# Optimization experiments

Hardware: AMD Instinct MI355X
Metric: run time of the kernel (lower is better)

## Reference

```python
import jax, jax.numpy as jnp
import numpy as np

NUM_HEADS = 16
EMBED_DIM = 2048
HEAD_DIM = EMBED_DIM // NUM_HEADS
B, S = 2, 2048


def setup_inputs() -> dict:
    key = jax.random.key(0)
    ks = jax.random.split(key, 12)
    E = EMBED_DIM
    scale = 1.0 / np.sqrt(E)  # xavier-ish for square E->E dense
    inp = {
        "x": jax.random.normal(ks[0], (B, S, E), dtype=jnp.float32),
        "sin": jax.random.uniform(ks[1], (1, NUM_HEADS, S, HEAD_DIM), dtype=jnp.float32),
        "cos": jax.random.uniform(ks[2], (1, NUM_HEADS, S, HEAD_DIM), dtype=jnp.float32),
        "mask": jax.random.randint(ks[3], (B, S, S), 0, 2, dtype=jnp.int32),
        "Wq": jax.random.normal(ks[4], (E, E), dtype=jnp.float32) * scale,
        "bq": jnp.zeros((E,), dtype=jnp.float32),
        "Wk": jax.random.normal(ks[5], (E, E), dtype=jnp.float32) * scale,
        "bk": jnp.zeros((E,), dtype=jnp.float32),
        "Wv": jax.random.normal(ks[6], (E, E), dtype=jnp.float32) * scale,
        "bv": jnp.zeros((E,), dtype=jnp.float32),
        "Wo": jax.random.normal(ks[7], (E, E), dtype=jnp.float32) * scale,
        "bo": jnp.zeros((E,), dtype=jnp.float32),
    }
    return inp


def _minus_swap_alternate(t):
    # stack([-t[...,1::2], t[...,::2]], -1).reshape(t.shape)
    return jnp.stack([-t[..., 1::2], t[..., ::2]], axis=-1).reshape(t.shape)


def _forward(x, sin, cos, mask, Wq, bq, Wk, bk, Wv, bv, Wo, bo):
    Bx, Sx, E = x.shape
    H, D = NUM_HEADS, HEAD_DIM
    q = (x @ Wq + bq).reshape(Bx, Sx, H, D).transpose(0, 2, 1, 3)  # (B,H,S,D)
    k = (x @ Wk + bk).reshape(Bx, Sx, H, D).transpose(0, 2, 1, 3)
    v = (x @ Wv + bv).reshape(Bx, Sx, H, D).transpose(0, 2, 1, 3)
    # RoPE applied post-transpose: T = q.shape[1] == H (faithful to source)
    T = q.shape[1]
    s = sin[:, :T, :, :]
    c = cos[:, :T, :, :]
    q = q * c + _minus_swap_alternate(q) * s
    k = k * c + _minus_swap_alternate(k) * s
    m = mask[:, None, :, :]  # expand_mask: (B,S,S) -> (B,1,S,S)
    logits = jnp.einsum("bhqd,bhkd->bhqk", q, k) / jnp.sqrt(jnp.float32(D))
    logits = jnp.where(m == 0, jnp.float32(-9e15), logits)
    attention = jax.nn.softmax(logits, axis=-1)          # first softmax
    values = jnp.matmul(attention, v)                    # (B,H,S,D)
    attention_weights = jax.nn.softmax(attention, axis=-1)  # redundant second softmax
    attn_output = jnp.matmul(attention_weights, values)  # (B,H,S,D)
    attn_output = attn_output.transpose(0, 2, 1, 3).reshape(Bx, Sx, E)
    out = attn_output @ Wo + bo
    return out, attention_weights


def reference(x, sin, cos, mask, Wq, bq, Wk, bk, Wv, bv, Wo, bo):
    return _forward(x, sin, cos, mask, Wq, bq, Wk, bk, Wv, bv, Wo, bo)
```

## Files before the change

kernel.cpp:

```cpp
#include <hip/hip_runtime.h>

typedef unsigned short u16;
typedef unsigned int u32;
typedef __attribute__((ext_vector_type(8))) short short8;
typedef __attribute__((ext_vector_type(4))) float floatx4;

constexpr int Bc = 2, Sc = 2048, Ec = 2048, Hc = 16, Dc = 128;
constexpr int TILE = 128, BK = 32;

__device__ __forceinline__ u16 f2bf(float f) {
  u32 u = __builtin_bit_cast(u32, f);
  u = (u + 0x7FFFu + ((u >> 16) & 1u)) >> 16;
  return (u16)u;
}

__device__ __forceinline__ short8 pack2(float4 a, float4 b) {
  short8 r;
  r[0] = (short)f2bf(a.x); r[1] = (short)f2bf(a.y);
  r[2] = (short)f2bf(a.z); r[3] = (short)f2bf(a.w);
  r[4] = (short)f2bf(b.x); r[5] = (short)f2bf(b.y);
  r[6] = (short)f2bf(b.z); r[7] = (short)f2bf(b.w);
  return r;
}

__device__ __forceinline__ void glds16(const u16* g, u16* l) {
  __builtin_amdgcn_global_load_lds(
      (const __attribute__((address_space(1))) u32*)g,
      (__attribute__((address_space(3))) u32*)l, 16, 0, 0);
}

__device__ __forceinline__ void gemm_core(const u16* __restrict__ A, int lda,
                                          const u16* __restrict__ Bt, int ldb,
                                          int K, int m0, int n0,
                                          u16* smA, u16* smB,
                                          floatx4 (*acc)[4]) {
  const int t = threadIdx.x;
  const int lane = t & 63;
  const int w = t >> 6;
  const int wr = (w >> 1) * 64, wc = (w & 1) * 64;
  const int l15 = lane & 15, q = lane >> 4;

  const int r0 = t >> 2;
  const int c0 = (t & 3) ^ (r0 & 3);
  const u16* A0 = A + (size_t)(m0 + r0) * lda + c0 * 8;
  const u16* A1 = A0 + (size_t)64 * lda;
  const u16* B0 = Bt + (size_t)(n0 + r0) * ldb + c0 * 8;
  const u16* B1 = B0 + (size_t)64 * ldb;
  u16* dA0 = smA + w * 512;
  u16* dA1 = smA + 2048 + w * 512;
  u16* dB0 = smB + w * 512;
  u16* dB1 = smB + 2048 + w * 512;

  for (int k0 = 0; k0 < K; k0 += BK) {
    glds16(A0 + k0, dA0);
    glds16(A1 + k0, dA1);
    glds16(B0 + k0, dB0);
    glds16(B1 + k0, dB1);
    __syncthreads();

    short8 af[4], bfr[4];
    #pragma unroll
    for (int i = 0; i < 4; i++) {
      int ra = wr + i * 16 + l15;
      af[i] = *(const short8*)&smA[ra * BK + ((q ^ (ra & 3)) << 3)];
      int rb = wc + i * 16 + l15;
      bfr[i] = *(const short8*)&smB[rb * BK + ((q ^ (rb & 3)) << 3)];
    }
    #pragma unroll
    for (int mi = 0; mi < 4; mi++)
      #pragma unroll
      for (int ni = 0; ni < 4; ni++)
        acc[mi][ni] = __builtin_amdgcn_mfma_f32_16x16x32_bf16(af[mi], bfr[ni], acc[mi][ni], 0, 0, 0);
    __syncthreads();
  }
}

__global__ __launch_bounds__(256) void transpose_w(
    const float* __restrict__ Wq, const float* __restrict__ Wk,
    const float* __restrict__ Wv, const float* __restrict__ Wo,
    u16* __restrict__ WT, u16* __restrict__ WoT) {
  __shared__ float tile[32][33];
  const int z = blockIdx.z;
  const float* W = (z == 0) ? Wq : (z == 1) ? Wk : (z == 2) ? Wv : Wo;
  u16* dst = (z < 3) ? (WT + (size_t)z * Ec * Ec) : WoT;
  const int n0 = blockIdx.x * 32, k0 = blockIdx.y * 32;
  const int tx = threadIdx.x, ty = threadIdx.y;
  #pragma unroll
  for (int i = 0; i < 4; i++)
    tile[ty + 8 * i][tx] = W[(size_t)(k0 + ty + 8 * i) * Ec + n0 + tx];
  __syncthreads();
  #pragma unroll
  for (int i = 0; i < 4; i++)
    dst[(size_t)(n0 + ty + 8 * i) * Ec + k0 + tx] = f2bf(tile[tx][ty + 8 * i]);
}

__global__ __launch_bounds__(256) void xcvt_kernel(const float* __restrict__ x,
                                                   u16* __restrict__ xb,
                                                   float* __restrict__ s1) {
  const int i = blockIdx.x * 256 + threadIdx.x;
  const float4 f0 = ((const float4*)x)[(size_t)i * 2];
  const float4 f1 = ((const float4*)x)[(size_t)i * 2 + 1];
  *(short8*)&xb[(size_t)i * 8] = pack2(f0, f1);
  if (blockIdx.x < 64)
    ((float4*)s1)[i] = make_float4(0.f, 0.f, 0.f, 0.f);
}

__global__ __launch_bounds__(256) void qkv_kernel(
    const u16* __restrict__ xb, const u16* __restrict__ WT,
    const float* __restrict__ bq, const float* __restrict__ bk, const float* __restrict__ bv,
    const float* __restrict__ sinp, const float* __restrict__ cosp,
    u16* __restrict__ qr, u16* __restrict__ kr, u16* __restrict__ vT) {
  __shared__ __align__(16) u16 smA[TILE * BK];
  __shared__ __align__(16) u16 smB[TILE * BK];
  floatx4 acc[4][4] = {};
  const int m0 = blockIdx.y * TILE, n0 = blockIdx.x * TILE;
  gemm_core(xb, Ec, WT, Ec, Ec, m0, n0, smA, smB, acc);

  const int t = threadIdx.x, lane = t & 63, w = t >> 6;
  const int wr = (w >> 1) * 64, wc = (w & 1) * 64, l15 = lane & 15, q = lane >> 4;
  #pragma unroll
  for (int mi = 0; mi < 4; mi++) {
    #pragma unroll
    for (int ni = 0; ni < 4; ni++) {
      const int gcol = n0 + wc + ni * 16 + l15;
      const int which = gcol >> 11;
      const int e = gcol & 2047, h = e >> 7, d = e & 127;
      const float* bp = (which == 0) ? bq : (which == 1) ? bk : bv;
      const float bias = bp[e];
      #pragma unroll
      for (int rr = 0; rr < 4; rr++) {
        const int grow = m0 + wr + mi * 16 + q * 4 + rr;
        const int b = grow >> 11, s = grow & 2047;
        float val = acc[mi][ni][rr] + bias;
        float pv = __shfl_xor(val, 1);
        if (which < 2) {
          const size_t sc = ((size_t)h * Sc + s) * Dc + d;
          const float c = cosp[sc], sn = sinp[sc];
          const float o = val * c + ((d & 1) ? pv : -pv) * sn;
          u16* dst = which ? kr : qr;
          dst[(((size_t)b * Hc + h) * Sc + s) * Dc + d] = f2bf(o);
        } else {
          vT[(((size_t)b * Hc + h) * Dc + d) * Sc + s] = f2bf(val);
        }
      }
    }
  }
}

__global__ __launch_bounds__(256) void logits_kernel(
    const u16* __restrict__ qr, const u16* __restrict__ kr,
    const int* __restrict__ maskp, float* __restrict__ Lo, float* __restrict__ s1) {
  __shared__ __align__(16) u16 smA[TILE * BK];
  __shared__ __align__(16) u16 smB[TILE * BK];
  floatx4 acc[4][4] = {};
  const int z = blockIdx.z;
  const int m0 = blockIdx.y * TILE, n0 = blockIdx.x * TILE;
  gemm_core(qr + (size_t)z * Sc * Dc, Dc, kr + (size_t)z * Sc * Dc, Dc, Dc, m0, n0, smA, smB, acc);

  float* C = Lo + (size_t)z * Sc * Sc;
  const int b = z >> 4;
  const float scale = 0.08838834764831845f;
  const int t = threadIdx.x, lane = t & 63, w = t >> 6;
  const int wr = (w >> 1) * 64, wc = (w & 1) * 64, l15 = lane & 15, q = lane >> 4;
  float rs[4][4];
  #pragma unroll
  for (int mi = 0; mi < 4; mi++)
    #pragma unroll
    for (int rr = 0; rr < 4; rr++) rs[mi][rr] = 0.f;

  #pragma unroll
  for (int mi = 0; mi < 4; mi++)
    #pragma unroll
    for (int ni = 0; ni < 4; ni++) {
      const int gcol = n0 + wc + ni * 16 + l15;
      #pragma unroll
      for (int rr = 0; rr < 4; rr++) {
        const int grow = m0 + wr + mi * 16 + q * 4 + rr;
        const int mv = maskp[((size_t)b * Sc + grow) * Sc + gcol];
        const float val = mv ? acc[mi][ni][rr] * scale : -9.0e15f;
        C[(size_t)grow * Sc + gcol] = val;
        rs[mi][rr] += __expf(val);
      }
    }
  #pragma unroll
  for (int mi = 0; mi < 4; mi++)
    #pragma unroll
    for (int rr = 0; rr < 4; rr++) {
      float xs = rs[mi][rr];
      xs += __shfl_xor(xs, 1);
      xs += __shfl_xor(xs, 2);
      xs += __shfl_xor(xs, 4);
      xs += __shfl_xor(xs, 8);
      if (l15 == 0)
        atomicAdd(&s1[z * Sc + m0 + wr + mi * 16 + q * 4 + rr], xs);
    }
}

__global__ __launch_bounds__(256) void av_kernel(
    const float* __restrict__ L, const u16* __restrict__ vT,
    const float* __restrict__ s1, u16* __restrict__ valT, float* __restrict__ s2) {
  __shared__ __align__(16) u16 smA[TILE * BK];
  __shared__ __align__(16) u16 smB[TILE * BK];
  floatx4 acc[4][4] = {};
  const int z = blockIdx.z;
  const int m0 = blockIdx.y * TILE;
  const int t = threadIdx.x;
  const int r = t >> 1, cg = (t & 1) * 2, sw = r & 3;
  const int lane = t & 63, w = t >> 6;
  const int wr = (w >> 1) * 64, wc = (w & 1) * 64;
  const int l15 = lane & 15, q = lane >> 4;

  const int r0 = t >> 2;
  const int c0 = (t & 3) ^ (r0 & 3);
  const u16* Bb = vT + (size_t)z * Dc * Sc;
  const u16* B0 = Bb + (size_t)r0 * Sc + c0 * 8;
  const u16* B1 = B0 + (size_t)64 * Sc;
  u16* dB0 = smB + w * 512;
  u16* dB1 = smB + 2048 + w * 512;

  const float* Arow = L + (size_t)z * Sc * Sc + (size_t)(m0 + r) * Sc + cg * 8;
  const float inv1 = 1.0f / s1[z * Sc + m0 + r];
  float s2p = 0.0f;

  for (int k0 = 0; k0 < Sc; k0 += BK) {
    glds16(B0 + k0, dB0);
    glds16(B1 + k0, dB1);

    float4 f[4];
    #pragma unroll
    for (int j = 0; j < 4; j++) f[j] = ((const float4*)(Arow + k0))[j];
    #pragma unroll
    for (int j = 0; j < 4; j++) {
      float* e = (float*)&f[j];
      #pragma unroll
      for (int u = 0; u < 4; u++) {
        float a1 = __expf(e[u]) * inv1;
        s2p += __expf(a1);
        e[u] = a1;
      }
    }
    short8 a0 = pack2(f[0], f[1]);
    short8 a1v = pack2(f[2], f[3]);
    *(short8*)&smA[r * BK + (((cg + 0) ^ sw) << 3)] = a0;
    *(short8*)&smA[r * BK + (((cg + 1) ^ sw) << 3)] = a1v;
    __syncthreads();

    short8 af[4], bfr[4];
    #pragma unroll
    for (int i = 0; i < 4; i++) {
      int ra = wr + i * 16 + l15;
      af[i] = *(const short8*)&smA[ra * BK + ((q ^ (ra & 3)) << 3)];
      int rb = wc + i * 16 + l15;
      bfr[i] = *(const short8*)&smB[rb * BK + ((q ^ (rb & 3)) << 3)];
    }
    #pragma unroll
    for (int mi = 0; mi < 4; mi++)
      #pragma unroll
      for (int ni = 0; ni < 4; ni++)
        acc[mi][ni] = __builtin_amdgcn_mfma_f32_16x16x32_bf16(af[mi], bfr[ni], acc[mi][ni], 0, 0, 0);
    __syncthreads();
  }

  float o = __shfl_xor(s2p, 1);
  if ((t & 1) == 0) s2[z * Sc + m0 + r] = s2p + o;

  u16* C = valT + (size_t)z * Dc * Sc;
  #pragma unroll
  for (int mi = 0; mi < 4; mi++)
    #pragma unroll
    for (int ni = 0; ni < 4; ni++) {
      const int gcol = wc + ni * 16 + l15;
      #pragma unroll
      for (int rr = 0; rr < 4; rr++) {
        const int grow = m0 + wr + mi * 16 + q * 4 + rr;
        C[(size_t)gcol * Sc + grow] = f2bf(acc[mi][ni][rr]);
      }
    }
}

__global__ __launch_bounds__(256) void wv_kernel(
    float* __restrict__ L, const u16* __restrict__ valT,
    const float* __restrict__ s1, const float* __restrict__ s2,
    u16* __restrict__ aox) {
  __shared__ __align__(16) u16 smA[TILE * BK];
  __shared__ __align__(16) u16 smB[TILE * BK];
  floatx4 acc[4][4] = {};
  const int z = blockIdx.z;
  const int m0 = blockIdx.y * TILE;
  const int t = threadIdx.x;
  const int r = t >> 1, cg = (t & 1) * 2, sw = r & 3;
  const int lane = t & 63, w = t >> 6;
  const int wr = (w >> 1) * 64, wc = (w & 1) * 64;
  const int l15 = lane & 15, q = lane >> 4;

  const int r0 = t >> 2;
  const int c0 = (t & 3) ^ (r0 & 3);
  const u16* Bb = valT + (size_t)z * Dc * Sc;
  const u16* B0 = Bb + (size_t)r0 * Sc + c0 * 8;
  const u16* B1 = B0 + (size_t)64 * Sc;
  u16* dB0 = smB + w * 512;
  u16* dB1 = smB + 2048 + w * 512;

  float* Arow = L + (size_t)z * Sc * Sc + (size_t)(m0 + r) * Sc + cg * 8;
  const float inv1 = 1.0f / s1[z * Sc + m0 + r];
  const float inv2 = 1.0f / s2[z * Sc + m0 + r];

  for (int k0 = 0; k0 < Sc; k0 += BK) {
    glds16(B0 + k0, dB0);
    glds16(B1 + k0, dB1);

    float4 f[4];
    #pragma unroll
    for (int j = 0; j < 4; j++) f[j] = ((const float4*)(Arow + k0))[j];
    #pragma unroll
    for (int j = 0; j < 4; j++) {
      float* e = (float*)&f[j];
      #pragma unroll
      for (int u = 0; u < 4; u++) {
        float a1 = __expf(e[u]) * inv1;
        e[u] = __expf(a1) * inv2;
      }
    }
    #pragma unroll
    for (int j = 0; j < 4; j++) ((float4*)(Arow + k0))[j] = f[j];
    short8 a0 = pack2(f[0], f[1]);
    short8 a1v = pack2(f[2], f[3]);
    *(short8*)&smA[r * BK + (((cg + 0) ^ sw) << 3)] = a0;
    *(short8*)&smA[r * BK + (((cg + 1) ^ sw) << 3)] = a1v;
    __syncthreads();

    short8 af[4], bfr[4];
    #pragma unroll
    for (int i = 0; i < 4; i++) {
      int ra = wr + i * 16 + l15;
      af[i] = *(const short8*)&smA[ra * BK + ((q ^ (ra & 3)) << 3)];
      int rb = wc + i * 16 + l15;
      bfr[i] = *(const short8*)&smB[rb * BK + ((q ^ (rb & 3)) << 3)];
    }
    #pragma unroll
    for (int mi = 0; mi < 4; mi++)
      #pragma unroll
      for (int ni = 0; ni < 4; ni++)
        acc[mi][ni] = __builtin_amdgcn_mfma_f32_16x16x32_bf16(af[mi], bfr[ni], acc[mi][ni], 0, 0, 0);
    __syncthreads();
  }

  const int b = z >> 4, h = z & 15;
  #pragma unroll
  for (int mi = 0; mi < 4; mi++)
    #pragma unroll
    for (int ni = 0; ni < 4; ni++) {
      const int gcol = wc + ni * 16 + l15;
      #pragma unroll
      for (int rr = 0; rr < 4; rr++) {
        const int grow = m0 + wr + mi * 16 + q * 4 + rr;
        aox[((size_t)b * Sc + grow) * Ec + h * Dc + gcol] = f2bf(acc[mi][ni][rr]);
      }
    }
}

__global__ __launch_bounds__(256) void out_kernel(
    const u16* __restrict__ aox, const u16* __restrict__ WoT,
    const float* __restrict__ bo, float* __restrict__ outp) {
  __shared__ __align__(16) u16 smA[TILE * BK];
  __shared__ __align__(16) u16 smB[TILE * BK];
  floatx4 acc[4][4] = {};
  const int m0 = blockIdx.y * TILE, n0 = blockIdx.x * TILE;
  gemm_core(aox, Ec, WoT, Ec, Ec, m0, n0, smA, smB, acc);

  const int t = threadIdx.x, lane = t & 63, w = t >> 6;
  const int wr = (w >> 1) * 64, wc = (w & 1) * 64, l15 = lane & 15, q = lane >> 4;
  #pragma unroll
  for (int mi = 0; mi < 4; mi++)
    #pragma unroll
    for (int ni = 0; ni < 4; ni++) {
      const int gcol = n0 + wc + ni * 16 + l15;
      const float bias = bo[gcol];
      #pragma unroll
      for (int rr = 0; rr < 4; rr++) {
        const int grow = m0 + wr + mi * 16 + q * 4 + rr;
        outp[(size_t)grow * Ec + gcol] = acc[mi][ni][rr] + bias;
      }
    }
}

extern "C" void kernel_launch(void* const* d_in, const int* in_sizes, int n_in,
                              void* d_out, int out_size, void* d_ws, size_t ws_size,
                              hipStream_t stream) {
  const float* x     = (const float*)d_in[0];
  const float* sinp  = (const float*)d_in[1];
  const float* cosp  = (const float*)d_in[2];
  const int*   maskp = (const int*)d_in[3];
  const float* Wq    = (const float*)d_in[4];
  const float* bq    = (const float*)d_in[5];
  const float* Wk    = (const float*)d_in[6];
  const float* bk    = (const float*)d_in[7];
  const float* Wv    = (const float*)d_in[8];
  const float* bv    = (const float*)d_in[9];
  const float* Wo    = (const float*)d_in[10];
  const float* bo    = (const float*)d_in[11];

  float* out0  = (float*)d_out;
  float* attnL = out0 + (size_t)Bc * Sc * Ec;

  u16* wsp  = (u16*)d_ws;
  u16* WT   = wsp;
  u16* WoT  = WT + (size_t)3 * Ec * Ec;
  u16* xb   = WoT + (size_t)Ec * Ec;
  u16* qr   = xb + (size_t)Bc * Sc * Ec;
  u16* kr   = qr + (size_t)Bc * Hc * Sc * Dc;
  u16* vT   = kr + (size_t)Bc * Hc * Sc * Dc;
  u16* valT = vT + (size_t)Bc * Hc * Sc * Dc;
  u16* aox  = valT + (size_t)Bc * Hc * Sc * Dc;
  float* s1 = (float*)(aox + (size_t)Bc * Sc * Ec);
  float* s2 = s1 + (size_t)Bc * Hc * Sc;

  transpose_w<<<dim3(64, 64, 4), dim3(32, 8), 0, stream>>>(Wq, Wk, Wv, Wo, WT, WoT);
  xcvt_kernel<<<dim3(4096), 256, 0, stream>>>(x, xb, s1);
  qkv_kernel<<<dim3(48, 32), 256, 0, stream>>>(xb, WT, bq, bk, bv, sinp, cosp, qr, kr, vT);
  logits_kernel<<<dim3(16, 16, 32), 256, 0, stream>>>(qr, kr, maskp, attnL, s1);
  av_kernel<<<dim3(1, 16, 32), 256, 0, stream>>>(attnL, vT, s1, valT, s2);
  wv_kernel<<<dim3(1, 16, 32), 256, 0, stream>>>(attnL, valT, s1, s2, aox);
  out_kernel<<<dim3(16, 32), 256, 0, stream>>>(aox, WoT, bo, out0);
}
```

Baseline: 1.466 ms.

## Store unnormalized exp scores as bf16 and defer softmax normalization to epilogue

The logits kernel now writes exp(logit) as bf16 into a workspace buffer instead of fp32 logits into the output. av_kernel loads this buffer straight into LDS with global_load_lds, multiplies by unnormalized P and applies 1/s1 in the epilogue, which removes the per-element exp work from its staging path. wv_kernel reads the bf16 buffer and writes the final fp32 attention weights. This halves the intermediate read traffic at the cost of an extra workspace buffer and bf16 rounding of exp values before normalization and the second softmax.

After: 1.304 ms. 11.0% less time.

```diff
diff --git a/kernel.cpp b/kernel.cpp
--- a/kernel.cpp
+++ b/kernel.cpp
@@ -12,6 +12,11 @@
   u32 u = __builtin_bit_cast(u32, f);
   u = (u + 0x7FFFu + ((u >> 16) & 1u)) >> 16;
   return (u16)u;
+}
+
+__device__ __forceinline__ float bf2f(short s) {
+  u32 u = ((u32)(u16)s) << 16;
+  return __builtin_bit_cast(float, u);
 }
 
 __device__ __forceinline__ short8 pack2(float4 a, float4 b) {
@@ -149,7 +154,7 @@
 
 __global__ __launch_bounds__(256) void logits_kernel(
     const u16* __restrict__ qr, const u16* __restrict__ kr,
-    const int* __restrict__ maskp, float* __restrict__ Lo, float* __restrict__ s1) {
+    const int* __restrict__ maskp, u16* __restrict__ Pbuf, float* __restrict__ s1) {
   __shared__ __align__(16) u16 smA[TILE * BK];
   __shared__ __align__(16) u16 smB[TILE * BK];
   floatx4 acc[4][4] = {};
@@ -157,7 +162,7 @@
   const int m0 = blockIdx.y * TILE, n0 = blockIdx.x * TILE;
   gemm_core(qr + (size_t)z * Sc * Dc, Dc, kr + (size_t)z * Sc * Dc, Dc, Dc, m0, n0, smA, smB, acc);
 
-  float* C = Lo + (size_t)z * Sc * Sc;
+  u16* Pp = Pbuf + (size_t)z * Sc * Sc;
   const int b = z >> 4;
   const float scale = 0.08838834764831845f;
   const int t = threadIdx.x, lane = t & 63, w = t >> 6;
@@ -178,8 +183,9 @@
         const int grow = m0 + wr + mi * 16 + q * 4 + rr;
         const int mv = maskp[((size_t)b * Sc + grow) * Sc + gcol];
         const float val = mv ? acc[mi][ni][rr] * scale : -9.0e15f;
-        C[(size_t)grow * Sc + gcol] = val;
-        rs[mi][rr] += __expf(val);
+        const float pe = __expf(val);
+        rs[mi][rr] += pe;
+        Pp[(size_t)grow * Sc + gcol] = f2bf(pe);
       }
     }
   #pragma unroll
@@ -197,8 +203,98 @@
 }
 
 __global__ __launch_bounds__(256) void av_kernel(
-    const float* __restrict__ L, const u16* __restrict__ vT,
+    const u16* __restrict__ P, const u16* __restrict__ vT,
     const float* __restrict__ s1, u16* __restrict__ valT, float* __restrict__ s2) {
+  __shared__ __align__(16) u16 smA[TILE * BK];
+  __shared__ __align__(16) u16 smB[TILE * BK];
+  floatx4 acc[4][4] = {};
+  const int z = blockIdx.z;
+  const int m0 = blockIdx.y * TILE;
+  const int t = threadIdx.x, lane = t & 63, w = t >> 6;
+  const int wr = (w >> 1) * 64, wc = (w & 1) * 64;
+  const int l15 = lane & 15, q = lane >> 4;
+
+  const int r0 = t >> 2;
+  const int c0 = (t & 3) ^ (r0 & 3);
+  const u16* Pb = P + (size_t)z * Sc * Sc;
+  const u16* A0 = Pb + (size_t)(m0 + r0) * Sc + c0 * 8;
+  const u16* A1 = A0 + (size_t)64 * Sc;
+  const u16* Bb = vT + (size_t)z * Dc * Sc;
+  const u16* B0 = Bb + (size_t)r0 * Sc + c0 * 8;
+  const u16* B1 = B0 + (size_t)64 * Sc;
+  u16* dA0 = smA + w * 512;
+  u16* dA1 = smA + 2048 + w * 512;
+  u16* dB0 = smB + w * 512;
+  u16* dB1 = smB + 2048 + w * 512;
+
+  const float inv1a = 1.0f / s1[z * Sc + m0 + r0];
+  const float inv1b = 1.0f / s1[z * Sc + m0 + r0 + 64];
+  float s2a = 0.0f, s2b = 0.0f;
+
+  for (int k0 = 0; k0 < Sc; k0 += BK) {
+    glds16(A0 + k0, dA0);
+    glds16(A1 + k0, dA1);
+    glds16(B0 + k0, dB0);
+    glds16(B1 + k0, dB1);
+    __syncthreads();
+
+    short8 af[4], bfr[4];
+    #pragma unroll
+    for (int i = 0; i < 4; i++) {
+      int ra = wr + i * 16 + l15;
+      af[i] = *(const short8*)&smA[ra * BK + ((q ^ (ra & 3)) << 3)];
+      int rb = wc + i * 16 + l15;
+      bfr[i] = *(const short8*)&smB[rb * BK + ((q ^ (rb & 3)) << 3)];
+    }
+    short8 pa = *(const short8*)&smA[t * 8];
+    short8 pb = *(const short8*)&smA[2048 + t * 8];
+
+    #pragma unroll
+    for (int mi = 0; mi < 4; mi++)
+      #pragma unroll
+      for (int ni = 0; ni < 4; ni++)
+        acc[mi][ni] = __builtin_amdgcn_mfma_f32_16x16x32_bf16(af[mi], bfr[ni], acc[mi][ni], 0, 0, 0);
+
+    #pragma unroll
+    for (int j = 0; j < 8; j++) {
+      s2a += __expf(bf2f(pa[j]) * inv1a);
+      s2b += __expf(bf2f(pb[j]) * inv1b);
+    }
+    __syncthreads();
+  }
+
+  s2a += __shfl_xor(s2a, 1); s2a += __shfl_xor(s2a, 2);
+  s2b += __shfl_xor(s2b, 1); s2b += __shfl_xor(s2b, 2);
+  if ((t & 3) == 0) {
+    s2[z * Sc + m0 + r0] = s2a;
+    s2[z * Sc + m0 + r0 + 64] = s2b;
+  }
+
+  float iv[4][4];
+  #pragma unroll
+  for (int mi = 0; mi < 4; mi++)
+    #pragma unroll
+    for (int rr = 0; rr < 4; rr++)
+      iv[mi][rr] = 1.0f / s1[z * Sc + m0 + wr + mi * 16 + q * 4 + rr];
+
+  u16* C = valT + (size_t)z * Dc * Sc;
+  #pragma unroll
+  for (int mi = 0; mi < 4; mi++)
+    #pragma unroll
+    for (int ni = 0; ni < 4; ni++) {
+      const int gcol = wc + ni * 16 + l15;
+      #pragma unroll
+      for (int rr = 0; rr < 4; rr++) {
+        const int grow = m0 + wr + mi * 16 + q * 4 + rr;
+        C[(size_t)gcol * Sc + grow] = f2bf(acc[mi][ni][rr] * iv[mi][rr]);
+      }
+    }
+}
+
+__global__ __launch_bounds__(256) void wv_kernel(
+    const u16* __restrict__ P, const u16* __restrict__ valT,
+    const float* __restrict__ s1, const float* __restrict__ s2,
+    float* __restrict__ a2out, u16* __restrict__ aox) {
   __shared__ __align__(16) u16 smA[TILE * BK];
   __shared__ __align__(16) u16 smB[TILE * BK];
   floatx4 acc[4][4] = {};
@@ -212,96 +308,14 @@
 
   const int r0 = t >> 2;
   const int c0 = (t & 3) ^ (r0 & 3);
-  const u16* Bb = vT + (size_t)z * Dc * Sc;
-  const u16* B0 = Bb + (size_t)r0 * Sc + c0 * 8;
-  const u16* B1 = B0 + (size_t)64 * Sc;
-  u16* dB0 = smB + w * 512;
-  u16* dB1 = smB + 2048 + w * 512;
-
-  const float* Arow = L + (size_t)z * Sc * Sc + (size_t)(m0 + r) * Sc + cg * 8;
-  const float inv1 = 1.0f / s1[z * Sc + m0 + r];
-  float s2p = 0.0f;
-
-  for (int k0 = 0; k0 < Sc; k0 += BK) {
-    glds16(B0 + k0, dB0);
-    glds16(B1 + k0, dB1);
-
-    float4 f[4];
-    #pragma unroll
-    for (int j = 0; j < 4; j++) f[j] = ((const float4*)(Arow + k0))[j];
-    #pragma unroll
-    for (int j = 0; j < 4; j++) {
-      float* e = (float*)&f[j];
-      #pragma unroll
-      for (int u = 0; u < 4; u++) {
-        float a1 = __expf(e[u]) * inv1;
-        s2p += __expf(a1);
-        e[u] = a1;
-      }
-    }
-    short8 a0 = pack2(f[0], f[1]);
-    short8 a1v = pack2(f[2], f[3]);
-    *(short8*)&smA[r * BK + (((cg + 0) ^ sw) << 3)] = a0;
-    *(short8*)&smA[r * BK + (((cg + 1) ^ sw) << 3)] = a1v;
-    __syncthreads();
-
-    short8 af[4], bfr[4];
-    #pragma unroll
-    for (int i = 0; i < 4; i++) {
-      int ra = wr + i * 16 + l15;
-      af[i] = *(const short8*)&smA[ra * BK + ((q ^ (ra & 3)) << 3)];
-      int rb = wc + i * 16 + l15;
-      bfr[i] = *(const short8*)&smB[rb * BK + ((q ^ (rb & 3)) << 3)];
-    }
-    #pragma unroll
-    for (int mi = 0; mi < 4; mi++)
-      #pragma unroll
-      for (int ni = 0; ni < 4; ni++)
-        acc[mi][ni] = __builtin_amdgcn_mfma_f32_16x16x32_bf16(af[mi], bfr[ni], acc[mi][ni], 0, 0, 0);
-    __syncthreads();
-  }
-
-  float o = __shfl_xor(s2p, 1);
-  if ((t & 1) == 0) s2[z * Sc + m0 + r] = s2p + o;
-
-  u16* C = valT + (size_t)z * Dc * Sc;
-  #pragma unroll
-  for (int mi = 0; mi < 4; mi++)
-    #pragma unroll
-    for (int ni = 0; ni < 4; ni++) {
-      const int gcol = wc + ni * 16 + l15;
-      #pragma unroll
-      for (int rr = 0; rr < 4; rr++) {
-        const int grow = m0 + wr + mi * 16 + q * 4 + rr;
-        C[(size_t)gcol * Sc + grow] = f2bf(acc[mi][ni][rr]);
-      }
-    }
-}
-
-__global__ __launch_bounds__(256) void wv_kernel(
-    float* __restrict__ L, const u16* __restrict__ valT,
-    const float* __restrict__ s1, const float* __restrict__ s2,
-    u16* __restrict__ aox) {
-  __shared__ __align__(16) u16 smA[TILE * BK];
-  __shared__ __align__(16) u16 smB[TILE * BK];
-  floatx4 acc[4][4] = {};
-  const int z = blockIdx.z;
-  const int m0 = blockIdx.y * TILE;
-  const int t = threadIdx.x;
-  const int r = t >> 1, cg = (t & 1) * 2, sw = r & 3;
-  const int lane = t & 63, w = t >> 6;
-  const int wr = (w >> 1) * 64, wc = (w & 1) * 64;
-  const int l15 = lane & 15, q = lane >> 4;
-
-  const int r0 = t >> 2;
-  const int c0 = (t & 3) ^ (r0 & 3);
   const u16* Bb = valT + (size_t)z * Dc * Sc;
   const u16* B0 = Bb + (size_t)r0 * Sc + c0 * 8;
   const u16* B1 = B0 + (size_t)64 * Sc;
   u16* dB0 = smB + w * 512;
   u16* dB1 = smB + 2048 + w * 512;
 
-  float* Arow = L + (size_t)z * Sc * Sc + (size_t)(m0 + r) * Sc + cg * 8;
+  const u16* Prow = P + (size_t)z * Sc * Sc + (size_t)(m0 + r) * Sc + cg * 8;
+  float* Orow = a2out + (size_t)z * Sc * Sc + (size_t)(m0 + r) * Sc + cg * 8;
   const float inv1 = 1.0f / s1[z * Sc + m0 + r];
   const float inv2 = 1.0f / s2[z * Sc + m0 + r];
 
@@ -309,20 +323,16 @@
     glds16(B0 + k0, dB0);
     glds16(B1 + k0, dB1);
 
+    short8 p0 = *(const short8*)(Prow + k0);
+    short8 p1 = *(const short8*)(Prow + k0 + 8);
     float4 f[4];
-    #pragma unroll
-    for (int j = 0; j < 4; j++) f[j] = ((const float4*)(Arow + k0))[j];
-    #pragma unroll
-    for (int j = 0; j < 4; j++) {
-      float* e = (float*)&f[j];
-      #pragma unroll
-      for (int u = 0; u < 4; u++) {
-        float a1 = __expf(e[u]) * inv1;
-        e[u] = __expf(a1) * inv2;
-      }
-    }
-    #pragma unroll
-    for (int j = 0; j < 4; j++) ((float4*)(Arow + k0))[j] = f[j];
+    float* e = (float*)f;
+    #pragma unroll
+    for (int j = 0; j < 8; j++) e[j] = __expf(bf2f(p0[j]) * inv1) * inv2;
+    #pragma unroll
+    for (int j = 0; j < 8; j++) e[8 + j] = __expf(bf2f(p1[j]) * inv1) * inv2;
+    #pragma unroll
+    for (int j = 0; j < 4; j++) ((float4*)(Orow + k0))[j] = f[j];
     short8 a0 = pack2(f[0], f[1]);
     short8 a1v = pack2(f[2], f[3]);
     *(short8*)&smA[r * BK + (((cg + 0) ^ sw) << 3)] = a0;
@@ -414,12 +424,13 @@
   u16* aox  = valT + (size_t)Bc * Hc * Sc * Dc;
   float* s1 = (float*)(aox + (size_t)Bc * Sc * Ec);
   float* s2 = s1 + (size_t)Bc * Hc * Sc;
+  u16* Pbuf = (u16*)(s2 + (size_t)Bc * Hc * Sc);
 
   transpose_w<<<dim3(64, 64, 4), dim3(32, 8), 0, stream>>>(Wq, Wk, Wv, Wo, WT, WoT);
   xcvt_kernel<<<dim3(4096), 256, 0, stream>>>(x, xb, s1);
   qkv_kernel<<<dim3(48, 32), 256, 0, stream>>>(xb, WT, bq, bk, bv, sinp, cosp, qr, kr, vT);
-  logits_kernel<<<dim3(16, 16, 32), 256, 0, stream>>>(qr, kr, maskp, attnL, s1);
-  av_kernel<<<dim3(1, 16, 32), 256, 0, stream>>>(attnL, vT, s1, valT, s2);
-  wv_kernel<<<dim3(1, 16, 32), 256, 0, stream>>>(attnL, valT, s1, s2, aox);
+  logits_kernel<<<dim3(16, 16, 32), 256, 0, stream>>>(qr, kr, maskp, Pbuf, s1);
+  av_kernel<<<dim3(1, 16, 32), 256, 0, stream>>>(Pbuf, vT, s1, valT, s2);
+  wv_kernel<<<dim3(1, 16, 32), 256, 0, stream>>>(Pbuf, valT, s1, s2, attnL, aox);
   out_kernel<<<dim3(16, 32), 256, 0, stream>>>(aox, WoT, bo, out0);
 }
```
